# Kernel optimization log

Measured on AMD Instinct MI355X. Metric: run time of the kernel, lower is better.

The kernel has to match this reference:

```python
import jax, jax.numpy as jnp
import numpy as np

# dims: P planes, N planar nodes/plane, M nexus nodes, E edges/plane, C classes
P, N, M, E, C, FP, FN = 3, 100000, 30000, 200000, 5, 64, 32


def class_linear(x, W, b):
    # x: [..., C, in], W: [C, out, in], b: [C, out] -> [..., C, out]
    return jnp.einsum('...ci,coi->...co', x, W) + b


def setup_inputs() -> dict:
    key = jax.random.key(0)
    ks = jax.random.split(key, 12)
    def nrm(k, shape, scale=1.0):
        return jax.random.normal(k, shape, jnp.float32) * scale
    return {
        'x': nrm(ks[0], (P, N, C, FP)),
        'nexus': nrm(ks[1], (M, C, FN)),
        'edge_src': jax.random.randint(ks[2], (P, E), 0, N, jnp.int32),
        'edge_dst': jax.random.randint(ks[3], (P, E), 0, M, jnp.int32),
        'Wn1': nrm(ks[4], (C, FN, P * FP), (P * FP) ** -0.5),
        'bn1': jnp.zeros((C, FN), jnp.float32),
        'Wn2': nrm(ks[5], (C, FN, FN), FN ** -0.5),
        'bn2': jnp.zeros((C, FN), jnp.float32),
        'We': nrm(ks[6], (P, C, 1, FP + FN), (FP + FN) ** -0.5),
        'be': jnp.zeros((P, C, 1), jnp.float32),
        'Wd1': nrm(ks[7], (P, C, FP, FP + FN), (FP + FN) ** -0.5),
        'bd1': jnp.zeros((P, C, FP), jnp.float32),
        'Wd2': nrm(ks[8], (P, C, FP, FP), FP ** -0.5),
        'bd2': jnp.zeros((P, C, FP), jnp.float32),
    }


def reference(x, nexus, edge_src, edge_dst, Wn1, bn1, Wn2, bn2,
              We, be, Wd1, bd1, Wd2, bd2):
    # --- nexus_up: SimpleConv (sum-aggregate planar features at nexus nodes) ---
    def up_one(xp, src, dst):
        return jax.ops.segment_sum(xp[src], dst, num_segments=M)  # [M,C,FP]
    up = jax.vmap(up_one)(x, edge_src, edge_dst)                   # [P,M,C,FP]
    # torch.cat(n, dim=-1) over planes -> [M, C, P*FP]
    n_cat = jnp.transpose(up, (1, 2, 0, 3)).reshape(M, C, P * FP)

    # --- nexus_net: ClassLinear -> tanh -> ClassLinear -> tanh ---
    n = jnp.tanh(class_linear(n_cat, Wn1, bn1))
    n = jnp.tanh(class_linear(n, Wn2, bn2))                        # [M,C,FN]

    # --- nexus_down per plane (flow target_to_source, aggr mean at src) ---
    def down_one(xp, src, dst, We_p, be_p, W1, b1, W2, b2):
        x_i = xp[src]                                              # [E,C,FP]
        n_j = n[dst]                                               # [E,C,FN]
        feat = jax.lax.stop_gradient(jnp.concatenate([x_i, n_j], -1))
        # per-class scalar logit, softmax over class dim (dim=1)
        w = jax.nn.softmax(class_linear(feat, We_p, be_p), axis=1)  # [E,C,1]
        msg = w * n_j                                               # [E,C,FN]
        s = jax.ops.segment_sum(msg, src, num_segments=N)           # [N,C,FN]
        cnt = jax.ops.segment_sum(jnp.ones((E,), msg.dtype), src, num_segments=N)
        aggr = s / jnp.maximum(cnt, 1.0)[:, None, None]             # scatter-mean
        h = jnp.tanh(class_linear(jnp.concatenate([xp, aggr], -1), W1, b1))
        return jnp.tanh(class_linear(h, W2, b2))                    # [N,C,FP]

    out = jax.vmap(down_one)(x, edge_src, edge_dst, We, be, Wd1, bd1, Wd2, bd2)
    return out  # [P,N,C,FP] updated planar embeddings (x['u'],x['v'],x['y'])
```

## Files before the change

### kernel.cpp

```cpp
#include <hip/hip_runtime.h>
#include <hip/hip_fp16.h>

#define P_ 3
#define N_ 100000
#define M_ 30000
#define E_ 200000
#define C_ 5
#define FP_ 64
#define FN_ 32
#define PFP_ 192
#define FPFN_ 96
#define PE_ 600000
#define PN_ 300000
#define PM_ 90000
#define NT_ 64
#define TILES_ ((N_ + NT_ - 1) / NT_)
#define NTD_ 64
#define TILESD_ ((N_ + NTD_ - 1) / NTD_)
#define CFN_ 160
#define NW1_ 92160
#define NW2_ 61440
#define NB_S_ ((PN_ + 1023) / 1024)
#define NB_D_ ((PM_ + 1023) / 1024)

typedef _Float16 f16x8 __attribute__((ext_vector_type(8)));
typedef float f32x4 __attribute__((ext_vector_type(4)));

__device__ __forceinline__ float fast_tanh(float v) {
  float x = fminf(fmaxf(v, -15.0f), 15.0f);
  float t = __expf(2.0f * x);
  return __fdividef(t - 1.0f, t + 1.0f);
}

__device__ __forceinline__ f16x8 ld8(const __half* p) {
  return *(const f16x8*)(const void*)p;
}

__global__ void k_count(const int* __restrict__ esrc, const int* __restrict__ edst,
                        int* __restrict__ cnt_src, int* __restrict__ cnt_dst) {
  int i = blockIdx.x * 256 + threadIdx.x;
  if (i >= PE_) return;
  int p = i / E_;
  atomicAdd(&cnt_src[p * N_ + esrc[i]], 1);
  atomicAdd(&cnt_dst[p * M_ + edst[i]], 1);
}

__global__ void k_scan1c(const int* __restrict__ in_s, int* __restrict__ out_s,
                         int* __restrict__ aux_s,
                         const int* __restrict__ in_d, int* __restrict__ out_d,
                         int* __restrict__ aux_d) {
  __shared__ int lds[256];
  int b = blockIdx.x, t = threadIdx.x;
  const int* in;
  int* out;
  int* aux;
  int n;
  if (b < NB_S_) { in = in_s; out = out_s; aux = aux_s; n = PN_; }
  else           { b -= NB_S_; in = in_d; out = out_d; aux = aux_d; n = PM_; }
  int base = b * 1024 + t * 4;
  int v0 = (base + 0 < n) ? in[base + 0] : 0;
  int v1 = (base + 1 < n) ? in[base + 1] : 0;
  int v2 = (base + 2 < n) ? in[base + 2] : 0;
  int v3 = (base + 3 < n) ? in[base + 3] : 0;
  lds[t] = v0 + v1 + v2 + v3;
  __syncthreads();
  for (int off = 1; off < 256; off <<= 1) {
    int xv = (t >= off) ? lds[t - off] : 0;
    __syncthreads();
    lds[t] += xv;
    __syncthreads();
  }
  if (t == 255) aux[b] = lds[255];
  int run = (t == 0) ? 0 : lds[t - 1];
  if (base + 0 < n) out[base + 0] = run; run += v0;
  if (base + 1 < n) out[base + 1] = run; run += v1;
  if (base + 2 < n) out[base + 2] = run; run += v2;
  if (base + 3 < n) out[base + 3] = run;
}

__global__ void k_scan2c(int* __restrict__ aux_s, int* __restrict__ end_s,
                         int* __restrict__ aux_d, int* __restrict__ end_d) {
  __shared__ int lds[1024];
  int t = threadIdx.x;
  int* aux = (blockIdx.x == 0) ? aux_s : aux_d;
  int* offe = (blockIdx.x == 0) ? end_s : end_d;
  int nb = (blockIdx.x == 0) ? NB_S_ : NB_D_;
  lds[t] = (t < nb) ? aux[t] : 0;
  __syncthreads();
  for (int off = 1; off < 1024; off <<= 1) {
    int xv = (t >= off) ? lds[t - off] : 0;
    __syncthreads();
    lds[t] += xv;
    __syncthreads();
  }
  if (t < nb) aux[t] = (t == 0) ? 0 : lds[t - 1];
  if (t == 0) offe[0] = lds[nb - 1];
}

__global__ void k_scan3c(int* __restrict__ off_s, const int* __restrict__ aux_s,
                         int* __restrict__ cur_s,
                         int* __restrict__ off_d, const int* __restrict__ aux_d,
                         int* __restrict__ cur_d) {
  int i = blockIdx.x * 256 + threadIdx.x;
  if (i < PN_) {
    int v = off_s[i] + aux_s[i >> 10];
    off_s[i] = v;
    cur_s[i] = v;
  } else if (i < PN_ + PM_) {
    int j = i - PN_;
    int v = off_d[j] + aux_d[j >> 10];
    off_d[j] = v;
    cur_d[j] = v;
  }
}

__global__ void k_fill(const int* __restrict__ esrc, const int* __restrict__ edst,
                       int* __restrict__ cur_src, int* __restrict__ cur_dst,
                       int* __restrict__ list_src, int* __restrict__ list_dst) {
  int i = blockIdx.x * 256 + threadIdx.x;
  if (i >= PE_) return;
  int p = i / E_;
  int s = esrc[i], d = edst[i];
  int ps = atomicAdd(&cur_src[p * N_ + s], 1);
  list_src[ps] = d;
  int pd = atomicAdd(&cur_dst[p * M_ + d], 1);
  list_dst[pd] = s;
}

__global__ void k_wconv(const float* __restrict__ Wd1, const float* __restrict__ Wd2,
                        __half* __restrict__ w1h, __half* __restrict__ w2h) {
  int i = blockIdx.x * 256 + threadIdx.x;
  if (i < NW1_) w1h[i] = __float2half(Wd1[i]);
  if (i < NW2_) w2h[i] = __float2half(Wd2[i]);
}

__global__ __launch_bounds__(320) void k_projx(
    const float* __restrict__ x, const float* __restrict__ Wn1,
    const float* __restrict__ We,
    __half* __restrict__ y, float* __restrict__ xdot,
    __half* __restrict__ xh, int write_xh) {
  __shared__ __align__(16) __half xs[NT_ * 320];
  int bp = blockIdx.x;
  int p = bp / TILES_, tile = bp % TILES_;
  int base = tile * NT_;
  int rows = min(NT_, N_ - base);
  int t = threadIdx.x;
  int g = t / CFN_, u = t % CFN_;
  int c = u >> 5;

  __half2 w[32];
  {
    const float* wr = &Wn1[(size_t)u * PFP_ + p * FP_];
    #pragma unroll
    for (int i = 0; i < 32; ++i) w[i] = __floats2half2_rn(wr[2*i], wr[2*i+1]);
  }

  const float* xb = x + (size_t)(p * N_ + base) * (C_ * FP_);
  int tot = rows * 320;
  for (int f = t * 4; f < tot; f += 320 * 4) {
    float4 v = *(const float4*)(xb + f);
    __half2* dst = (__half2*)&xs[f];
    dst[0] = __floats2half2_rn(v.x, v.y);
    dst[1] = __floats2half2_rn(v.z, v.w);
  }
  __syncthreads();

  if (write_xh) {
    __half* xo = xh + (size_t)(p * N_ + base) * 320;
    for (int f = t * 8; f < tot; f += 320 * 8)
      *(float4*)&xo[f] = *(const float4*)&xs[f];
  }

  for (int r = g; r < rows; r += 2) {
    const __half2* xr = (const __half2*)&xs[r * 320 + c * FP_];
    __half2 acc = __floats2half2_rn(0.f, 0.f);
    #pragma unroll
    for (int i = 0; i < 32; ++i) acc = __hfma2(xr[i], w[i], acc);
    float s = __low2float(acc) + __high2float(acc);
    y[(size_t)(p * N_ + base + r) * CFN_ + u] = __float2half(s);
  }

  {
    int cx = t >> 6, nodex = t & 63;
    if (nodex < rows) {
      const __half2* xr = (const __half2*)&xs[nodex * 320 + cx * FP_];
      const float2* wer = (const float2*)&We[(p * C_ + cx) * FPFN_];
      float s = 0.f;
      #pragma unroll
      for (int i = 0; i < 32; ++i) {
        float2 wv = wer[i];
        __half2 xv = xr[i];
        s += __low2float(xv) * wv.x + __high2float(xv) * wv.y;
      }
      xdot[(size_t)(p * N_ + base + nodex) * C_ + cx] = s;
    }
  }
}

__global__ __launch_bounds__(320) void k_nexus(
    const __half* __restrict__ y,
    const int* __restrict__ off_dst, const int* __restrict__ list_dst,
    const float* __restrict__ bn1,
    const float* __restrict__ Wn2, const float* __restrict__ bn2,
    const float* __restrict__ We,
    __half* __restrict__ nout, float* __restrict__ ndot) {
  __shared__ float part[4][CFN_];
  __shared__ __align__(16) float h1S[CFN_];
  __shared__ __align__(16) float h2S[CFN_];
  int m = blockIdx.x;
  int t = threadIdx.x;
  int g = t / 80, u2 = t % 80;

  float afx = 0.f, afy = 0.f;
  #pragma unroll
  for (int p = 0; p < P_; ++p) {
    int o0 = off_dst[p * M_ + m];
    int o1 = off_dst[p * M_ + m + 1];
    const __half2* yp2 = (const __half2*)(y + (size_t)p * N_ * CFN_);
    for (int e0 = o0 + g; e0 < o1; e0 += 8) {
      int e1 = e0 + 4;
      int s0 = list_dst[e0];
      int s1 = list_dst[e1 < o1 ? e1 : e0];
      __half2 v0 = yp2[(size_t)s0 * 80 + u2];
      __half2 v1 = yp2[(size_t)s1 * 80 + u2];
      afx += __low2float(v0); afy += __high2float(v0);
      if (e1 < o1) { afx += __low2float(v1); afy += __high2float(v1); }
    }
  }
  part[g][2 * u2]     = afx;
  part[g][2 * u2 + 1] = afy;
  __syncthreads();
  if (t < CFN_) {
    float pre = part[0][t] + part[1][t] + part[2][t] + part[3][t] + bn1[t];
    h1S[t] = fast_tanh(pre);
  }
  __syncthreads();
  if (t < CFN_) {
    int c = t >> 5;
    const float4* f4 = (const float4*)&h1S[c * FN_];
    const float4* w4 = (const float4*)&Wn2[(size_t)t * FN_];
    float a = bn2[t];
    #pragma unroll
    for (int i = 0; i < FN_ / 4; ++i) {
      float4 f = f4[i], wv = w4[i];
      a += f.x * wv.x + f.y * wv.y + f.z * wv.z + f.w * wv.w;
    }
    float nv = fast_tanh(a);
    h2S[t] = nv;
    nout[(size_t)m * CFN_ + t] = __float2half(nv);
  }
  __syncthreads();
  if (t < P_ * C_) {
    int p = t / C_, cc = t % C_;
    const float* wv = &We[(p * C_ + cc) * FPFN_ + FP_];
    float a = 0.f;
    #pragma unroll
    for (int j = 0; j < FN_; ++j) a += h2S[cc * FN_ + j] * wv[j];
    ndot[(size_t)(p * M_ + m) * C_ + cc] = a;
  }
}

template<int XH>
__global__ __launch_bounds__(128, 6) void k_dec(
    const float* __restrict__ x, const __half* __restrict__ xh,
    const __half* __restrict__ nout, const float* __restrict__ ndot,
    const float* __restrict__ xdot, const float* __restrict__ be,
    const int* __restrict__ off_src, const int* __restrict__ list_src,
    const __half* __restrict__ w1h, const float* __restrict__ bd1,
    const __half* __restrict__ w2h, const float* __restrict__ bd2,
    float* __restrict__ out) {
  __shared__ __align__(16) __half featS[NTD_ * 104];

  int bp = blockIdx.x;
  int pc = bp / TILESD_;
  int tile = bp % TILESD_;
  int p = pc / C_, c = pc % C_;
  int base = tile * NTD_;
  int rows = min(NTD_, N_ - base);

  int t = threadIdx.x;
  int w = t >> 6, l = t & 63;
  int l15 = l & 15, l4 = l >> 4;

  if constexpr (XH) {
    for (int idx = t; idx < NTD_ * 8; idx += 128) {
      int node = idx >> 3, q = idx & 7;
      if (node < rows) {
        float4 v = *(const float4*)&xh[(size_t)(p * N_ + base + node) * 320 + c * 64 + q * 8];
        *(float4*)&featS[node * 104 + q * 8] = v;
      }
    }
  } else {
    for (int idx = t; idx < NTD_ * 16; idx += 128) {
      int node = idx >> 4, fq = idx & 15;
      if (node < rows) {
        float4 v = *(const float4*)&x[(size_t)(p * N_ + base + node) * 320 + c * 64 + fq * 4];
        __half2* dst = (__half2*)&featS[node * 104 + fq * 4];
        dst[0] = __floats2half2_rn(v.x, v.y);
        dst[1] = __floats2half2_rn(v.z, v.w);
      }
    }
  }
  {
    int nd = t >> 1, hf = t & 1;
    if (nd < rows) {
      int pn = p * N_ + base + nd;
      int o0 = off_src[pn], o1 = off_src[pn + 1];
      float base_c[C_];
      #pragma unroll
      for (int cc = 0; cc < C_; ++cc)
        base_c[cc] = xdot[(size_t)pn * C_ + cc] + be[p * C_ + cc];
      float acc[16];
      #pragma unroll
      for (int i = 0; i < 16; ++i) acc[i] = 0.f;
      for (int e = o0; e < o1; ++e) {
        int dst = list_src[e];
        const float* nd5 = &ndot[(size_t)(p * M_ + dst) * C_];
        float lg[C_];
        #pragma unroll
        for (int cc = 0; cc < C_; ++cc) lg[cc] = base_c[cc] + nd5[cc];
        float mx = fmaxf(fmaxf(fmaxf(lg[0], lg[1]), fmaxf(lg[2], lg[3])), lg[4]);
        float s = 0.f;
        #pragma unroll
        for (int cc = 0; cc < C_; ++cc) { lg[cc] = __expf(lg[cc] - mx); s += lg[cc]; }
        float wgt = __fdividef(lg[c], s);
        const __half2* nr = (const __half2*)&nout[(size_t)dst * CFN_ + c * FN_ + hf * 16];
        #pragma unroll
        for (int i = 0; i < 8; ++i) {
          __half2 v = nr[i];
          acc[2 * i]     += wgt * __low2float(v);
          acc[2 * i + 1] += wgt * __high2float(v);
        }
      }
      float invd = __fdividef(1.0f, fmaxf((float)(o1 - o0), 1.0f));
      __half2* dst2 = (__half2*)&featS[nd * 104 + 64 + hf * 16];
      #pragma unroll
      for (int i = 0; i < 8; ++i)
        dst2[i] = __floats2half2_rn(acc[2 * i] * invd, acc[2 * i + 1] * invd);
    }
  }
  __syncthreads();

  int rbase = w * 32;
  const __half* w1g = w1h + (size_t)(p * C_ + c) * 64 * 96;
  const __half* w2g = w2h + (size_t)(p * C_ + c) * 64 * 64;

  f32x4 acc[2][4];
  #pragma unroll
  for (int tt = 0; tt < 4; ++tt) {
    float bv = bd1[(p * C_ + c) * FP_ + tt * 16 + l15];
    #pragma unroll
    for (int rt = 0; rt < 2; ++rt) acc[rt][tt] = (f32x4){bv, bv, bv, bv};
  }
  #pragma unroll
  for (int s = 0; s < 3; ++s) {
    f16x8 a0 = ld8(&featS[(rbase + l15) * 104 + s * 32 + l4 * 8]);
    f16x8 a1 = ld8(&featS[(rbase + 16 + l15) * 104 + s * 32 + l4 * 8]);
    #pragma unroll
    for (int tt = 0; tt < 4; ++tt) {
      f16x8 b = ld8(&w1g[(tt * 16 + l15) * 96 + s * 32 + l4 * 8]);
      acc[0][tt] = __builtin_amdgcn_mfma_f32_16x16x32_f16(a0, b, acc[0][tt], 0, 0, 0);
      acc[1][tt] = __builtin_amdgcn_mfma_f32_16x16x32_f16(a1, b, acc[1][tt], 0, 0, 0);
    }
  }
  #pragma unroll
  for (int rt = 0; rt < 2; ++rt)
    #pragma unroll
    for (int tt = 0; tt < 4; ++tt) {
      #pragma unroll
      for (int r = 0; r < 4; ++r) {
        int nrow = rbase + rt * 16 + l4 * 4 + r;
        featS[nrow * 104 + tt * 16 + l15] = __float2half(fast_tanh(acc[rt][tt][r]));
      }
    }

  f32x4 acc2[2][4];
  #pragma unroll
  for (int tt = 0; tt < 4; ++tt) {
    float bv = bd2[(p * C_ + c) * FP_ + tt * 16 + l15];
    #pragma unroll
    for (int rt = 0; rt < 2; ++rt) acc2[rt][tt] = (f32x4){bv, bv, bv, bv};
  }
  #pragma unroll
  for (int s = 0; s < 2; ++s) {
    f16x8 a0 = ld8(&featS[(rbase + l15) * 104 + s * 32 + l4 * 8]);
    f16x8 a1 = ld8(&featS[(rbase + 16 + l15) * 104 + s * 32 + l4 * 8]);
    #pragma unroll
    for (int tt = 0; tt < 4; ++tt) {
      f16x8 b = ld8(&w2g[(tt * 16 + l15) * 64 + s * 32 + l4 * 8]);
      acc2[0][tt] = __builtin_amdgcn_mfma_f32_16x16x32_f16(a0, b, acc2[0][tt], 0, 0, 0);
      acc2[1][tt] = __builtin_amdgcn_mfma_f32_16x16x32_f16(a1, b, acc2[1][tt], 0, 0, 0);
    }
  }
  #pragma unroll
  for (int rt = 0; rt < 2; ++rt)
    #pragma unroll
    for (int tt = 0; tt < 4; ++tt) {
      #pragma unroll
      for (int r = 0; r < 4; ++r) {
        int nrow = rbase + rt * 16 + l4 * 4 + r;
        int node = base + nrow;
        if (node < N_) {
          out[(size_t)(p * N_ + node) * 320 + c * 64 + tt * 16 + l15] =
              fast_tanh(acc2[rt][tt][r]);
        }
      }
    }
}

#define WS_Y     0ll
#define WS_NOUT  24000000ll
#define WS_XDOT  28800000ll
#define WS_NDOT  30300000ll
#define WS_OFFS  30750000ll
#define WS_OFFD  31050001ll
#define WS_CURS  31140002ll
#define WS_CURD  31440002ll
#define WS_LISTS 31530002ll
#define WS_LISTD 32130002ll
#define WS_AUX1  32730002ll
#define WS_AUX2  32730514ll
#define WS_W1H   32731026ll
#define WS_W2H   32777106ll
#define WS_XH    32808000ll
#define WS_XH_END_BYTES ((WS_XH + 48000000ll) * 4ll)

extern "C" void kernel_launch(void* const* d_in, const int* in_sizes, int n_in,
                              void* d_out, int out_size, void* d_ws, size_t ws_size,
                              hipStream_t stream) {
  const float* x   = (const float*)d_in[0];
  const int* esrc  = (const int*)d_in[2];
  const int* edst  = (const int*)d_in[3];
  const float* Wn1 = (const float*)d_in[4];
  const float* bn1 = (const float*)d_in[5];
  const float* Wn2 = (const float*)d_in[6];
  const float* bn2 = (const float*)d_in[7];
  const float* We  = (const float*)d_in[8];
  const float* be  = (const float*)d_in[9];
  const float* Wd1 = (const float*)d_in[10];
  const float* bd1 = (const float*)d_in[11];
  const float* Wd2 = (const float*)d_in[12];
  const float* bd2 = (const float*)d_in[13];
  float* out = (float*)d_out;

  float* wsf = (float*)d_ws;
  int*   wsi = (int*)d_ws;
  __half* ybuf = (__half*)d_ws;
  __half* nout = (__half*)(wsi + WS_NOUT);
  float* xdot = wsf + WS_XDOT;
  float* ndot = wsf + WS_NDOT;
  int* off_src = wsi + WS_OFFS;
  int* off_dst = wsi + WS_OFFD;
  int* cur_src = wsi + WS_CURS;
  int* cur_dst = wsi + WS_CURD;
  int* list_src = wsi + WS_LISTS;
  int* list_dst = wsi + WS_LISTD;
  int* aux1 = wsi + WS_AUX1;
  int* aux2 = wsi + WS_AUX2;
  __half* w1h = (__half*)(wsi + WS_W1H);
  __half* w2h = (__half*)(wsi + WS_W2H);
  __half* xh  = (__half*)(wsi + WS_XH);

  int use_xh = (ws_size >= (size_t)WS_XH_END_BYTES) ? 1 : 0;

  k_wconv<<<(NW1_ + 255) / 256, 256, 0, stream>>>(Wd1, Wd2, w1h, w2h);

  hipMemsetAsync(cur_src, 0, (PN_ + PM_) * sizeof(int), stream);
  k_count<<<(PE_ + 255) / 256, 256, 0, stream>>>(esrc, edst, cur_src, cur_dst);
  k_scan1c<<<NB_S_ + NB_D_, 256, 0, stream>>>(cur_src, off_src, aux1,
                                              cur_dst, off_dst, aux2);
  k_scan2c<<<2, 1024, 0, stream>>>(aux1, off_src + PN_, aux2, off_dst + PM_);
  k_scan3c<<<(PN_ + PM_ + 255) / 256, 256, 0, stream>>>(off_src, aux1, cur_src,
                                                        off_dst, aux2, cur_dst);
  k_fill<<<(PE_ + 255) / 256, 256, 0, stream>>>(esrc, edst, cur_src, cur_dst,
                                                list_src, list_dst);

  k_projx<<<P_ * TILES_, 320, 0, stream>>>(x, Wn1, We, ybuf, xdot, xh, use_xh);
  k_nexus<<<M_, 320, 0, stream>>>(ybuf, off_dst, list_dst, bn1, Wn2, bn2, We,
                                  nout, ndot);
  if (use_xh) {
    k_dec<1><<<P_ * C_ * TILESD_, 128, 0, stream>>>(x, xh, nout, ndot, xdot, be,
                                                    off_src, list_src,
                                                    w1h, bd1, w2h, bd2, out);
  } else {
    k_dec<0><<<P_ * C_ * TILESD_, 128, 0, stream>>>(x, xh, nout, ndot, xdot, be,
                                                    off_src, list_src,
                                                    w1h, bd1, w2h, bd2, out);
  }
}
```

Before: 857.8 us.

## Precompute per-edge softmax weights in nexus kernel and merge setup kernels

Merges the count kernel with the weight fp16 conversion, and the CSR fill kernel with the x projection kernel, so fewer launches are issued. Per-edge class softmax weights are now computed once per edge inside the nexus kernel, using edge-index lists built during fill, and stored as fp16. The decoder, which previously recomputed the 5-way softmax for each of the 5 class blocks, now just loads one weight. This adds edge-id lists, a weight buffer, and extra gather traffic, and the weights lose precision by going through fp16.

After: 838.6 us. 1.02x faster.

```diff
diff --git a/kernel.cpp b/kernel.cpp
--- a/kernel.cpp
+++ b/kernel.cpp
@@ -22,6 +22,10 @@
 #define NW2_ 61440
 #define NB_S_ ((PN_ + 1023) / 1024)
 #define NB_D_ ((PM_ + 1023) / 1024)
+#define NB_CNT_ ((PE_ + 255) / 256)
+#define NB_WC_ ((NW1_ + 255) / 256)
+#define NB_PROJ_ (P_ * TILES_)
+#define NB_FILL_ ((PE_ + 319) / 320)
 
 typedef _Float16 f16x8 __attribute__((ext_vector_type(8)));
 typedef float f32x4 __attribute__((ext_vector_type(4)));
@@ -36,13 +40,22 @@
   return *(const f16x8*)(const void*)p;
 }
 
-__global__ void k_count(const int* __restrict__ esrc, const int* __restrict__ edst,
-                        int* __restrict__ cnt_src, int* __restrict__ cnt_dst) {
-  int i = blockIdx.x * 256 + threadIdx.x;
-  if (i >= PE_) return;
-  int p = i / E_;
-  atomicAdd(&cnt_src[p * N_ + esrc[i]], 1);
-  atomicAdd(&cnt_dst[p * M_ + edst[i]], 1);
+__global__ void k_countw(const int* __restrict__ esrc, const int* __restrict__ edst,
+                         int* __restrict__ cnt_src, int* __restrict__ cnt_dst,
+                         const float* __restrict__ Wd1, const float* __restrict__ Wd2,
+                         __half* __restrict__ w1h, __half* __restrict__ w2h) {
+  int b = blockIdx.x;
+  if (b < NB_CNT_) {
+    int i = b * 256 + threadIdx.x;
+    if (i >= PE_) return;
+    int p = i / E_;
+    atomicAdd(&cnt_src[p * N_ + esrc[i]], 1);
+    atomicAdd(&cnt_dst[p * M_ + edst[i]], 1);
+  } else {
+    int i = (b - NB_CNT_) * 256 + threadIdx.x;
+    if (i < NW1_) w1h[i] = __float2half(Wd1[i]);
+    if (i < NW2_) w2h[i] = __float2half(Wd2[i]);
+  }
 }
 
 __global__ void k_scan1c(const int* __restrict__ in_s, int* __restrict__ out_s,
@@ -114,37 +127,37 @@
   }
 }
 
-__global__ void k_fill(const int* __restrict__ esrc, const int* __restrict__ edst,
-                       int* __restrict__ cur_src, int* __restrict__ cur_dst,
-                       int* __restrict__ list_src, int* __restrict__ list_dst) {
-  int i = blockIdx.x * 256 + threadIdx.x;
-  if (i >= PE_) return;
-  int p = i / E_;
-  int s = esrc[i], d = edst[i];
-  int ps = atomicAdd(&cur_src[p * N_ + s], 1);
-  list_src[ps] = d;
-  int pd = atomicAdd(&cur_dst[p * M_ + d], 1);
-  list_dst[pd] = s;
-}
-
-__global__ void k_wconv(const float* __restrict__ Wd1, const float* __restrict__ Wd2,
-                        __half* __restrict__ w1h, __half* __restrict__ w2h) {
-  int i = blockIdx.x * 256 + threadIdx.x;
-  if (i < NW1_) w1h[i] = __float2half(Wd1[i]);
-  if (i < NW2_) w2h[i] = __float2half(Wd2[i]);
-}
-
-__global__ __launch_bounds__(320) void k_projx(
+__global__ __launch_bounds__(320) void k_projfill(
     const float* __restrict__ x, const float* __restrict__ Wn1,
     const float* __restrict__ We,
     __half* __restrict__ y, float* __restrict__ xdot,
-    __half* __restrict__ xh, int write_xh) {
+    __half* __restrict__ xh, int write_xh,
+    const int* __restrict__ esrc, const int* __restrict__ edst,
+    int* __restrict__ cur_src, int* __restrict__ cur_dst,
+    int* __restrict__ list_src, int* __restrict__ list_src_e,
+    int* __restrict__ list_dst, int* __restrict__ list_dst_e) {
   __shared__ __align__(16) __half xs[NT_ * 320];
   int bp = blockIdx.x;
+  int t = threadIdx.x;
+
+  if (bp >= NB_PROJ_) {
+    int i = (bp - NB_PROJ_) * 320 + t;
+    if (i < PE_) {
+      int p = i / E_;
+      int s = esrc[i], d = edst[i];
+      int ps = atomicAdd(&cur_src[p * N_ + s], 1);
+      list_src[ps] = d;
+      list_src_e[ps] = i;
+      int pd = atomicAdd(&cur_dst[p * M_ + d], 1);
+      list_dst[pd] = s;
+      list_dst_e[pd] = i;
+    }
+    return;
+  }
+
   int p = bp / TILES_, tile = bp % TILES_;
   int base = tile * NT_;
   int rows = min(NT_, N_ - base);
-  int t = threadIdx.x;
   int g = t / CFN_, u = t % CFN_;
   int c = u >> 5;
 
@@ -200,13 +213,17 @@
 __global__ __launch_bounds__(320) void k_nexus(
     const __half* __restrict__ y,
     const int* __restrict__ off_dst, const int* __restrict__ list_dst,
+    const int* __restrict__ list_dst_e, const int* __restrict__ esrc,
     const float* __restrict__ bn1,
     const float* __restrict__ Wn2, const float* __restrict__ bn2,
     const float* __restrict__ We,
-    __half* __restrict__ nout, float* __restrict__ ndot) {
+    const float* __restrict__ xdot, const float* __restrict__ be,
+    __half* __restrict__ nout, __half* __restrict__ wbuf) {
   __shared__ float part[4][CFN_];
   __shared__ __align__(16) float h1S[CFN_];
   __shared__ __align__(16) float h2S[CFN_];
+  __shared__ float ndS[P_ * C_];
+  __shared__ float beS[P_ * C_];
   int m = blockIdx.x;
   int t = threadIdx.x;
   int g = t / 80, u2 = t % 80;
@@ -256,16 +273,39 @@
     float a = 0.f;
     #pragma unroll
     for (int j = 0; j < FN_; ++j) a += h2S[cc * FN_ + j] * wv[j];
-    ndot[(size_t)(p * M_ + m) * C_ + cc] = a;
+    ndS[t] = a;
+    beS[t] = be[t];
+  }
+  __syncthreads();
+  #pragma unroll
+  for (int p = 0; p < P_; ++p) {
+    int o0 = off_dst[p * M_ + m];
+    int o1 = off_dst[p * M_ + m + 1];
+    for (int e = o0 + t; e < o1; e += 320) {
+      int i = list_dst_e[e];
+      int src = esrc[i];
+      const float* xd = &xdot[(size_t)(p * N_ + src) * C_];
+      float lg[C_];
+      #pragma unroll
+      for (int cc = 0; cc < C_; ++cc) lg[cc] = xd[cc] + ndS[p * C_ + cc] + beS[p * C_ + cc];
+      float mx = fmaxf(fmaxf(fmaxf(lg[0], lg[1]), fmaxf(lg[2], lg[3])), lg[4]);
+      float s = 0.f;
+      #pragma unroll
+      for (int cc = 0; cc < C_; ++cc) { lg[cc] = __expf(lg[cc] - mx); s += lg[cc]; }
+      float inv = __fdividef(1.0f, s);
+      __half* wp = &wbuf[(size_t)i * C_];
+      #pragma unroll
+      for (int cc = 0; cc < C_; ++cc) wp[cc] = __float2half(lg[cc] * inv);
+    }
   }
 }
 
 template<int XH>
 __global__ __launch_bounds__(128, 6) void k_dec(
     const float* __restrict__ x, const __half* __restrict__ xh,
-    const __half* __restrict__ nout, const float* __restrict__ ndot,
-    const float* __restrict__ xdot, const float* __restrict__ be,
+    const __half* __restrict__ nout, const __half* __restrict__ wbuf,
     const int* __restrict__ off_src, const int* __restrict__ list_src,
+    const int* __restrict__ list_src_e,
     const __half* __restrict__ w1h, const float* __restrict__ bd1,
     const __half* __restrict__ w2h, const float* __restrict__ bd2,
     float* __restrict__ out) {
@@ -306,24 +346,13 @@
     if (nd < rows) {
       int pn = p * N_ + base + nd;
       int o0 = off_src[pn], o1 = off_src[pn + 1];
-      float base_c[C_];
-      #pragma unroll
-      for (int cc = 0; cc < C_; ++cc)
-        base_c[cc] = xdot[(size_t)pn * C_ + cc] + be[p * C_ + cc];
       float acc[16];
       #pragma unroll
       for (int i = 0; i < 16; ++i) acc[i] = 0.f;
       for (int e = o0; e < o1; ++e) {
         int dst = list_src[e];
-        const float* nd5 = &ndot[(size_t)(p * M_ + dst) * C_];
-        float lg[C_];
-        #pragma unroll
-        for (int cc = 0; cc < C_; ++cc) lg[cc] = base_c[cc] + nd5[cc];
-        float mx = fmaxf(fmaxf(fmaxf(lg[0], lg[1]), fmaxf(lg[2], lg[3])), lg[4]);
-        float s = 0.f;
-        #pragma unroll
-        for (int cc = 0; cc < C_; ++cc) { lg[cc] = __expf(lg[cc] - mx); s += lg[cc]; }
-        float wgt = __fdividef(lg[c], s);
+        int ie = list_src_e[e];
+        float wgt = __half2float(wbuf[(size_t)ie * C_ + c]);
         const __half2* nr = (const __half2*)&nout[(size_t)dst * CFN_ + c * FN_ + hf * 16];
         #pragma unroll
         for (int i = 0; i < 8; ++i) {
@@ -408,21 +437,24 @@
     }
 }
 
-#define WS_Y     0ll
-#define WS_NOUT  24000000ll
-#define WS_XDOT  28800000ll
-#define WS_NDOT  30300000ll
-#define WS_OFFS  30750000ll
-#define WS_OFFD  31050001ll
-#define WS_CURS  31140002ll
-#define WS_CURD  31440002ll
-#define WS_LISTS 31530002ll
-#define WS_LISTD 32130002ll
-#define WS_AUX1  32730002ll
-#define WS_AUX2  32730514ll
-#define WS_W1H   32731026ll
-#define WS_W2H   32777106ll
-#define WS_XH    32808000ll
+#define WS_Y      0ll
+#define WS_NOUT   24000000ll
+#define WS_LISTSE 26400000ll
+#define WS_WBUF   27000000ll
+#define WS_XDOT   28800000ll
+#define WS_NDOT   30300000ll
+#define WS_OFFS   30750000ll
+#define WS_OFFD   31050001ll
+#define WS_CURS   31140002ll
+#define WS_CURD   31440002ll
+#define WS_LISTS  31530002ll
+#define WS_LISTD  32130002ll
+#define WS_AUX1   32730002ll
+#define WS_AUX2   32730514ll
+#define WS_W1H    32731026ll
+#define WS_W2H    32777106ll
+#define WS_LISTDE 32808000ll
+#define WS_XH     33408000ll
 #define WS_XH_END_BYTES ((WS_XH + 48000000ll) * 4ll)
 
 extern "C" void kernel_launch(void* const* d_in, const int* in_sizes, int n_in,
@@ -447,14 +479,16 @@
   int*   wsi = (int*)d_ws;
   __half* ybuf = (__half*)d_ws;
   __half* nout = (__half*)(wsi + WS_NOUT);
+  __half* wbuf = (__half*)(wsi + WS_WBUF);
   float* xdot = wsf + WS_XDOT;
-  float* ndot = wsf + WS_NDOT;
   int* off_src = wsi + WS_OFFS;
   int* off_dst = wsi + WS_OFFD;
   int* cur_src = wsi + WS_CURS;
   int* cur_dst = wsi + WS_CURD;
   int* list_src = wsi + WS_LISTS;
+  int* list_src_e = wsi + WS_LISTSE;
   int* list_dst = wsi + WS_LISTD;
+  int* list_dst_e = wsi + WS_LISTDE;
   int* aux1 = wsi + WS_AUX1;
   int* aux2 = wsi + WS_AUX2;
   __half* w1h = (__half*)(wsi + WS_W1H);
@@ -463,28 +497,30 @@
 
   int use_xh = (ws_size >= (size_t)WS_XH_END_BYTES) ? 1 : 0;
 
-  k_wconv<<<(NW1_ + 255) / 256, 256, 0, stream>>>(Wd1, Wd2, w1h, w2h);
-
   hipMemsetAsync(cur_src, 0, (PN_ + PM_) * sizeof(int), stream);
-  k_count<<<(PE_ + 255) / 256, 256, 0, stream>>>(esrc, edst, cur_src, cur_dst);
+  k_countw<<<NB_CNT_ + NB_WC_, 256, 0, stream>>>(esrc, edst, cur_src, cur_dst,
+                                                 Wd1, Wd2, w1h, w2h);
   k_scan1c<<<NB_S_ + NB_D_, 256, 0, stream>>>(cur_src, off_src, aux1,
                                               cur_dst, off_dst, aux2);
   k_scan2c<<<2, 1024, 0, stream>>>(aux1, off_src + PN_, aux2, off_dst + PM_);
   k_scan3c<<<(PN_ + PM_ + 255) / 256, 256, 0, stream>>>(off_src, aux1, cur_src,
                                                         off_dst, aux2, cur_dst);
-  k_fill<<<(PE_ + 255) / 256, 256, 0, stream>>>(esrc, edst, cur_src, cur_dst,
-                                                list_src, list_dst);
-
-  k_projx<<<P_ * TILES_, 320, 0, stream>>>(x, Wn1, We, ybuf, xdot, xh, use_xh);
-  k_nexus<<<M_, 320, 0, stream>>>(ybuf, off_dst, list_dst, bn1, Wn2, bn2, We,
-                                  nout, ndot);
+
+  k_projfill<<<NB_PROJ_ + NB_FILL_, 320, 0, stream>>>(
+      x, Wn1, We, ybuf, xdot, xh, use_xh,
+      esrc, edst, cur_src, cur_dst,
+      list_src, list_src_e, list_dst, list_dst_e);
+
+  k_nexus<<<M_, 320, 0, stream>>>(ybuf, off_dst, list_dst, list_dst_e, esrc,
+                                  bn1, Wn2, bn2, We, xdot, be, nout, wbuf);
+
   if (use_xh) {
-    k_dec<1><<<P_ * C_ * TILESD_, 128, 0, stream>>>(x, xh, nout, ndot, xdot, be,
-                                                    off_src, list_src,
+    k_dec<1><<<P_ * C_ * TILESD_, 128, 0, stream>>>(x, xh, nout, wbuf,
+                                                    off_src, list_src, list_src_e,
                                                     w1h, bd1, w2h, bd2, out);
   } else {
-    k_dec<0><<<P_ * C_ * TILESD_, 128, 0, stream>>>(x, xh, nout, ndot, xdot, be,
-                                                    off_src, list_src,
+    k_dec<0><<<P_ * C_ * TILESD_, 128, 0, stream>>>(x, xh, nout, wbuf,
+                                                    off_src, list_src, list_src_e,
                                                     w1h, bd1, w2h, bd2, out);
   }
 }
```
